# Kernel tuning notes

Hardware: AMD Instinct MI355X
Metric: run time of the kernel (lower is better)

## Reference

```python
import jax, jax.numpy as jnp
import numpy as np

D_IN = 4096
D_OUT = 4096
EPS_NORM = 1e-6
EPS_Q = 1e-8


def _ternary_quantize(w):
    # per-output-channel absmean scale, then round/clamp to {-1,0,1}
    gamma = jnp.mean(jnp.abs(w), axis=-1)
    w_q = jnp.clip(jnp.round(w / (gamma[:, None] + EPS_Q)), -1.0, 1.0)
    return w_q, gamma


def setup_inputs() -> dict:
    key = jax.random.key(0)
    kx, kw = jax.random.split(key)
    x = jax.random.normal(kx, (2, 4096, D_IN), dtype=jnp.float32)
    # kaiming-uniform-like init then ternarize (mirrors torch __init__)
    bound = 1.0 / np.sqrt(D_IN)
    w_init = jax.random.uniform(kw, (D_OUT, D_IN), minval=-bound, maxval=bound, dtype=jnp.float32)
    w_q, gamma = _ternary_quantize(w_init)
    norm_weight = jnp.ones((D_IN,), dtype=jnp.float32)
    return {"x": x, "norm_weight": norm_weight, "w_q": w_q, "gamma": gamma}


def reference(x, norm_weight, w_q, gamma):
    # RMSNorm
    rms = jnp.sqrt(jnp.mean(x * x, axis=-1, keepdims=True) + EPS_NORM)
    xn = x / rms * norm_weight
    # ternary linear (dense fp32 GEMM, math identical to F.linear) + per-channel scale
    y = jnp.einsum('bsd,od->bso', xn, w_q) * gamma
    return y
```

## Files before the change

kernel.cpp:

```cpp
#include <hip/hip_runtime.h>
#include <hip/hip_bf16.h>
#include <stdint.h>

#define D_IN  4096
#define D_OUT 4096
#define MROWS 8192

using i32x4 = __attribute__((ext_vector_type(4))) int;

__global__ __launch_bounds__(256) void prep_kernel(
    const float* __restrict__ x, const float* __restrict__ nw,
    signed char* __restrict__ xq, float* __restrict__ srow,
    const float* __restrict__ wq, signed char* __restrict__ wb) {
  const int b = blockIdx.x;
  const int t = threadIdx.x;

  if (b < MROWS) {
    const float4* xr  = (const float4*)(x + (size_t)b * D_IN);
    const float4* nw4 = (const float4*)nw;

    float4 p[4];
    float ss = 0.f, mx = 0.f;
#pragma unroll
    for (int i = 0; i < 4; ++i) {
      const float4 v = xr[i * 256 + t];
      const float4 w = nw4[i * 256 + t];
      ss += v.x * v.x + v.y * v.y + v.z * v.z + v.w * v.w;
      p[i].x = v.x * w.x; p[i].y = v.y * w.y;
      p[i].z = v.z * w.z; p[i].w = v.w * w.w;
      mx = fmaxf(mx, fmaxf(fmaxf(fabsf(p[i].x), fabsf(p[i].y)),
                           fmaxf(fabsf(p[i].z), fabsf(p[i].w))));
    }
#pragma unroll
    for (int off = 32; off > 0; off >>= 1) {
      ss += __shfl_down(ss, off, 64);
      mx = fmaxf(mx, __shfl_down(mx, off, 64));
    }

    __shared__ float rs[4], rm[4];
    if ((t & 63) == 0) { rs[t >> 6] = ss; rm[t >> 6] = mx; }
    __syncthreads();
    const float scale =
        rsqrtf((rs[0] + rs[1] + rs[2] + rs[3]) * (1.0f / D_IN) + 1e-6f);
    const float rowmax = fmaxf(fmaxf(rm[0], rm[1]), fmaxf(rm[2], rm[3])) * scale;
    const float s   = fmaxf(rowmax, 1e-20f) * (1.0f / 127.0f);
    const float f   = scale / s;
    if (t == 0) srow[b] = s;

    int* out = (int*)(xq + (size_t)b * D_IN);
#pragma unroll
    for (int i = 0; i < 4; ++i) {
      const int q0 = (int)rintf(p[i].x * f);
      const int q1 = (int)rintf(p[i].y * f);
      const int q2 = (int)rintf(p[i].z * f);
      const int q3 = (int)rintf(p[i].w * f);
      out[i * 256 + t] =
          (q0 & 0xFF) | ((q1 & 0xFF) << 8) | ((q2 & 0xFF) << 16) | (q3 << 24);
    }
  } else {
    const int cb = b - MROWS;
    const float4* w4 = (const float4*)wq;
    int* o = (int*)wb;
#pragma unroll
    for (int i = 0; i < 4; ++i) {
      const int idx = cb * 1024 + i * 256 + t;
      const float4 v = w4[idx];
      const int q0 = (int)v.x, q1 = (int)v.y, q2 = (int)v.z, q3 = (int)v.w;
      o[idx] = (q0 & 0xFF) | ((q1 & 0xFF) << 8) | ((q2 & 0xFF) << 16) | (q3 << 24);
    }
  }
}

#define BM 256
#define BN 256
#define BKB 64
#define NKT (D_IN / BKB)
#define SLOT_BYTES (BM * BKB)

#define WVM(n_) asm volatile("s_waitcnt vmcnt(" #n_ ")" ::: "memory")
#define BAR()   __builtin_amdgcn_s_barrier()

#define STAGE(t_, s_)                                                         \
  do {                                                                        \
    const int _k0 = (t_) * BKB;                                               \
    _Pragma("unroll") for (int _i = 0; _i < 2; ++_i)                          \
        __builtin_amdgcn_global_load_lds(                                     \
            (__attribute__((address_space(1))) void*)(A + aOff[_i] + _k0),    \
            (__attribute__((address_space(3))) void*)&sA[s_][ldsOff[_i]],     \
            16, 0, 0);                                                        \
    _Pragma("unroll") for (int _i = 0; _i < 2; ++_i)                          \
        __builtin_amdgcn_global_load_lds(                                     \
            (__attribute__((address_space(1))) void*)(B + bOff[_i] + _k0),    \
            (__attribute__((address_space(3))) void*)&sB[s_][ldsOff[_i]],     \
            16, 0, 0);                                                        \
  } while (0)

#define COMPUTE(s_)                                                           \
  do {                                                                        \
    i32x4 af[8], bfr[4];                                                      \
    _Pragma("unroll") for (int _i = 0; _i < 8; ++_i)                          \
        af[_i] = *(const i32x4*)&sA[s_][aoff + _i * (16 * BKB)];              \
    _Pragma("unroll") for (int _j = 0; _j < 4; ++_j)                          \
        bfr[_j] = *(const i32x4*)&sB[s_][boff + _j * (16 * BKB)];             \
    __builtin_amdgcn_s_setprio(1);                                            \
    _Pragma("unroll") for (int _i = 0; _i < 8; ++_i)                          \
        _Pragma("unroll") for (int _j = 0; _j < 4; ++_j)                      \
            acc[_i][_j] = __builtin_amdgcn_mfma_i32_16x16x64_i8(              \
                af[_i], bfr[_j], acc[_i][_j], 0, 0, 0);                       \
    __builtin_amdgcn_s_setprio(0);                                            \
  } while (0)

__global__ __launch_bounds__(512, 2) void gemm_kernel(
    const signed char* __restrict__ A,
    const signed char* __restrict__ B,
    const float* __restrict__ srow,
    const float* __restrict__ gamma,
    float* __restrict__ C) {
  __shared__ __align__(16) signed char sA[4][SLOT_BYTES];
  __shared__ __align__(16) signed char sB[4][SLOT_BYTES];

  const int tid  = threadIdx.x;
  const int lane = tid & 63;
  const int wv   = tid >> 6;
  const int wm   = wv >> 2;
  const int wn   = wv & 3;
  const int bn   = blockIdx.x;
  const int bm   = blockIdx.y;

  i32x4 acc[8][4];
#pragma unroll
  for (int i = 0; i < 8; ++i)
#pragma unroll
    for (int j = 0; j < 4; ++j) acc[i][j] = (i32x4){0, 0, 0, 0};

  size_t aOff[2], bOff[2];
  int ldsOff[2];
#pragma unroll
  for (int i = 0; i < 2; ++i) {
    const int c  = i * 512 + tid;
    const int r  = c >> 2;
    const int cc = ((c & 3) ^ ((r >> 1) & 3)) * 16;
    aOff[i] = (size_t)(bm * BM + r) * D_IN + cc;
    bOff[i] = (size_t)(bn * BN + r) * D_IN + cc;
    ldsOff[i] = (i * 512 + wv * 64) * 16;
  }

  const int kk   = (((lane >> 4) ^ ((lane >> 1) & 3))) * 16;
  const int aoff = (wm * 128 + (lane & 15)) * BKB + kk;
  const int boff = (wn * 64  + (lane & 15)) * BKB + kk;

  STAGE(0, 0);
  STAGE(1, 1);
  STAGE(2, 2);
  WVM(8);
  BAR();

#pragma unroll 1
  for (int t4 = 0; t4 < NKT - 4; t4 += 4) {
    STAGE(t4 + 3, 3); COMPUTE(0); WVM(8); BAR();
    STAGE(t4 + 4, 0); COMPUTE(1); WVM(8); BAR();
    STAGE(t4 + 5, 1); COMPUTE(2); WVM(8); BAR();
    STAGE(t4 + 6, 2); COMPUTE(3); WVM(8); BAR();
  }
  STAGE(NKT - 1, 3); COMPUTE(0); WVM(8); BAR();
  COMPUTE(1); WVM(4); BAR();
  COMPUTE(2); WVM(0); BAR();
  COMPUTE(3);

  const int col0 = bn * BN + wn * 64 + (lane & 15);
  const int row0 = bm * BM + wm * 128 + ((lane >> 4) * 4);
  float g[4];
#pragma unroll
  for (int j = 0; j < 4; ++j) g[j] = gamma[col0 + j * 16];

#pragma unroll
  for (int i = 0; i < 8; ++i) {
#pragma unroll
    for (int r = 0; r < 4; ++r) {
      const int row = row0 + i * 16 + r;
      const float sr = srow[row];
#pragma unroll
      for (int j = 0; j < 4; ++j) {
        C[(size_t)row * D_OUT + col0 + j * 16] =
            (float)acc[i][j][r] * sr * g[j];
      }
    }
  }
}

#undef STAGE
#undef COMPUTE
#undef WVM
#undef BAR

extern "C" void kernel_launch(void* const* d_in, const int* in_sizes, int n_in,
                              void* d_out, int out_size, void* d_ws, size_t ws_size,
                              hipStream_t stream) {
  const float* x     = (const float*)d_in[0];
  const float* nw    = (const float*)d_in[1];
  const float* wq    = (const float*)d_in[2];
  const float* gamma = (const float*)d_in[3];
  float* y = (float*)d_out;

  signed char* xq = (signed char*)d_ws;
  signed char* wb = xq + (size_t)MROWS * D_IN;
  float* srow = (float*)(wb + (size_t)D_OUT * D_IN);

  prep_kernel<<<MROWS + 4096, 256, 0, stream>>>(x, nw, xq, srow, wq, wb);

  gemm_kernel<<<dim3(D_OUT / BN, MROWS / BM), 512, 0, stream>>>(xq, wb, srow, gamma, y);
}
```

Baseline: 388.0 us.

## Switch GEMM to 3-stage LDS ring with split-phase reads and interleaved loads

Replaces the 4-slot, 4x-unrolled prefetch pipeline with a 3-slot rotating ring. Each k-tile is split into two halves, with LDS fragment reads, A/B global-to-LDS loads and barriers interleaved between the two MFMA halves. This cuts LDS use from 128KB to 96KB per block and spreads memory issue across the compute phase. The cost is one less stage of prefetch depth, four barriers per tile instead of one, and runtime slot indices in place of constant ones.

```diff
diff --git a/kernel.cpp b/kernel.cpp
--- a/kernel.cpp
+++ b/kernel.cpp
@@ -80,34 +80,61 @@
 #define WVM(n_) asm volatile("s_waitcnt vmcnt(" #n_ ")" ::: "memory")
 #define BAR()   __builtin_amdgcn_s_barrier()
 
-#define STAGE(t_, s_)                                                         \
-  do {                                                                        \
-    const int _k0 = (t_) * BKB;                                               \
+#define STG_A(k0_, ss_)                                                       \
+  do {                                                                        \
     _Pragma("unroll") for (int _i = 0; _i < 2; ++_i)                          \
         __builtin_amdgcn_global_load_lds(                                     \
-            (__attribute__((address_space(1))) void*)(A + aOff[_i] + _k0),    \
-            (__attribute__((address_space(3))) void*)&sA[s_][ldsOff[_i]],     \
+            (__attribute__((address_space(1))) void*)(A + aOff[_i] + (k0_)),  \
+            (__attribute__((address_space(3))) void*)&sA[ss_][ldsOff[_i]],    \
             16, 0, 0);                                                        \
+  } while (0)
+#define STG_B(k0_, ss_)                                                       \
+  do {                                                                        \
     _Pragma("unroll") for (int _i = 0; _i < 2; ++_i)                          \
         __builtin_amdgcn_global_load_lds(                                     \
-            (__attribute__((address_space(1))) void*)(B + bOff[_i] + _k0),    \
-            (__attribute__((address_space(3))) void*)&sB[s_][ldsOff[_i]],     \
+            (__attribute__((address_space(1))) void*)(B + bOff[_i] + (k0_)),  \
+            (__attribute__((address_space(3))) void*)&sB[ss_][ldsOff[_i]],    \
             16, 0, 0);                                                        \
   } while (0)
 
-#define COMPUTE(s_)                                                           \
-  do {                                                                        \
-    i32x4 af[8], bfr[4];                                                      \
-    _Pragma("unroll") for (int _i = 0; _i < 8; ++_i)                          \
-        af[_i] = *(const i32x4*)&sA[s_][aoff + _i * (16 * BKB)];              \
+#define READ_P1()                                                             \
+  do {                                                                        \
+    _Pragma("unroll") for (int _i = 0; _i < 4; ++_i)                          \
+        af[_i] = *(const i32x4*)&sA[sC][aoff + _i * (16 * BKB)];              \
     _Pragma("unroll") for (int _j = 0; _j < 4; ++_j)                          \
-        bfr[_j] = *(const i32x4*)&sB[s_][boff + _j * (16 * BKB)];             \
+        bf[_j] = *(const i32x4*)&sB[sC][boff + _j * (16 * BKB)];              \
+  } while (0)
+#define READ_P2()                                                             \
+  do {                                                                        \
+    _Pragma("unroll") for (int _i = 0; _i < 4; ++_i)                          \
+        af[4 + _i] = *(const i32x4*)&sA[sC][aoff + (4 + _i) * (16 * BKB)];    \
+  } while (0)
+
+#define MFMA_HALF(base_)                                                      \
+  do {                                                                        \
     __builtin_amdgcn_s_setprio(1);                                            \
-    _Pragma("unroll") for (int _i = 0; _i < 8; ++_i)                          \
+    _Pragma("unroll") for (int _i = 0; _i < 4; ++_i)                          \
         _Pragma("unroll") for (int _j = 0; _j < 4; ++_j)                      \
-            acc[_i][_j] = __builtin_amdgcn_mfma_i32_16x16x64_i8(              \
-                af[_i], bfr[_j], acc[_i][_j], 0, 0, 0);                       \
+            acc[(base_) + _i][_j] = __builtin_amdgcn_mfma_i32_16x16x64_i8(    \
+                af[(base_) + _i], bf[_j], acc[(base_) + _i][_j], 0, 0, 0);    \
     __builtin_amdgcn_s_setprio(0);                                            \
+  } while (0)
+
+#define TILE_BODY(STGA_, STGB_, WAIT_)                                        \
+  do {                                                                        \
+    i32x4 af[8], bf[4];                                                       \
+    READ_P1();                                                                \
+    STGA_;                                                                    \
+    BAR();                                                                    \
+    MFMA_HALF(0);                                                             \
+    BAR();                                                                    \
+    READ_P2();                                                                \
+    STGB_;                                                                    \
+    BAR();                                                                    \
+    MFMA_HALF(4);                                                             \
+    WAIT_;                                                                    \
+    BAR();                                                                    \
+    const int _t = sC; sC = sN; sN = sS; sS = _t;                             \
   } while (0)
 
 __global__ __launch_bounds__(512, 2) void gemm_kernel(
@@ -116,8 +143,8 @@
     const float* __restrict__ srow,
     const float* __restrict__ gamma,
     float* __restrict__ C) {
-  __shared__ __align__(16) signed char sA[4][SLOT_BYTES];
-  __shared__ __align__(16) signed char sB[4][SLOT_BYTES];
+  __shared__ __align__(16) signed char sA[3][SLOT_BYTES];
+  __shared__ __align__(16) signed char sB[3][SLOT_BYTES];
 
   const int tid  = threadIdx.x;
   const int lane = tid & 63;
@@ -149,23 +176,20 @@
   const int aoff = (wm * 128 + (lane & 15)) * BKB + kk;
   const int boff = (wn * 64  + (lane & 15)) * BKB + kk;
 
-  STAGE(0, 0);
-  STAGE(1, 1);
-  STAGE(2, 2);
-  WVM(8);
+  int sC = 0, sN = 1, sS = 2;
+
+  STG_A(0, 0); STG_B(0, 0);
+  STG_A(BKB, 1); STG_B(BKB, 1);
+  WVM(4);
   BAR();
 
 #pragma unroll 1
-  for (int t4 = 0; t4 < NKT - 4; t4 += 4) {
-    STAGE(t4 + 3, 3); COMPUTE(0); WVM(8); BAR();
-    STAGE(t4 + 4, 0); COMPUTE(1); WVM(8); BAR();
-    STAGE(t4 + 5, 1); COMPUTE(2); WVM(8); BAR();
-    STAGE(t4 + 6, 2); COMPUTE(3); WVM(8); BAR();
-  }
-  STAGE(NKT - 1, 3); COMPUTE(0); WVM(8); BAR();
-  COMPUTE(1); WVM(4); BAR();
-  COMPUTE(2); WVM(0); BAR();
-  COMPUTE(3);
+  for (int T = 0; T < NKT - 2; ++T) {
+    const int k2 = (T + 2) * BKB;
+    TILE_BODY(STG_A(k2, sS), STG_B(k2, sS), WVM(4));
+  }
+  TILE_BODY(, , WVM(0));
+  TILE_BODY(, , );
 
   const int col0 = bn * BN + wn * 64 + (lane & 15);
   const int row0 = bm * BM + wm * 128 + ((lane >> 4) * 4);
@@ -188,8 +212,12 @@
   }
 }
 
-#undef STAGE
-#undef COMPUTE
+#undef TILE_BODY
+#undef MFMA_HALF
+#undef READ_P1
+#undef READ_P2
+#undef STG_A
+#undef STG_B
 #undef WVM
 #undef BAR
 
```

Measured after the change: 425.9 us. 9.8% more time.

## Widen K tile to 128 bytes with double-buffered LDS pipeline

Applied to the files above, without the earlier changes.

Doubles the K-step per stage to 128 int8 values and replaces the 4-slot, 3-deep prefetch pipeline with a 2-slot double buffer that waits for all loads (vmcnt 0) every iteration. The LDS swizzle is changed to an 8-way XOR pattern to match the wider rows. The aim is to halve the number of barriers and loop iterations per K tile. In exchange, prefetch depth drops from about three tiles to one, and the full wait each iteration can expose global load latency.

```diff
diff --git a/kernel.cpp b/kernel.cpp
--- a/kernel.cpp
+++ b/kernel.cpp
@@ -73,40 +73,40 @@
 
 #define BM 256
 #define BN 256
-#define BKB 64
+#define BKB 128
 #define NKT (D_IN / BKB)
 #define SLOT_BYTES (BM * BKB)
 
 #define WVM(n_) asm volatile("s_waitcnt vmcnt(" #n_ ")" ::: "memory")
 #define BAR()   __builtin_amdgcn_s_barrier()
 
-#define STAGE(t_, s_)                                                         \
+#define STAGE(k0_, ss_)                                                       \
   do {                                                                        \
-    const int _k0 = (t_) * BKB;                                               \
-    _Pragma("unroll") for (int _i = 0; _i < 2; ++_i)                          \
+    _Pragma("unroll") for (int _i = 0; _i < 4; ++_i)                          \
         __builtin_amdgcn_global_load_lds(                                     \
-            (__attribute__((address_space(1))) void*)(A + aOff[_i] + _k0),    \
-            (__attribute__((address_space(3))) void*)&sA[s_][ldsOff[_i]],     \
+            (__attribute__((address_space(1))) void*)(A + aOff[_i] + (k0_)),  \
+            (__attribute__((address_space(3))) void*)&sA[ss_][ldsOff[_i]],    \
             16, 0, 0);                                                        \
-    _Pragma("unroll") for (int _i = 0; _i < 2; ++_i)                          \
+    _Pragma("unroll") for (int _i = 0; _i < 4; ++_i)                          \
         __builtin_amdgcn_global_load_lds(                                     \
-            (__attribute__((address_space(1))) void*)(B + bOff[_i] + _k0),    \
-            (__attribute__((address_space(3))) void*)&sB[s_][ldsOff[_i]],     \
+            (__attribute__((address_space(1))) void*)(B + bOff[_i] + (k0_)),  \
+            (__attribute__((address_space(3))) void*)&sB[ss_][ldsOff[_i]],    \
             16, 0, 0);                                                        \
   } while (0)
 
-#define COMPUTE(s_)                                                           \
+#define COMPUTE_K(s_, kk_)                                                    \
   do {                                                                        \
-    i32x4 af[8], bfr[4];                                                      \
+    i32x4 af[8], bf[4];                                                       \
+    const int _ks = (((kk_)*4 + kx) ^ sx) * 16;                               \
     _Pragma("unroll") for (int _i = 0; _i < 8; ++_i)                          \
-        af[_i] = *(const i32x4*)&sA[s_][aoff + _i * (16 * BKB)];              \
+        af[_i] = *(const i32x4*)&sA[s_][aoff0 + _i * (16 * BKB) + _ks];       \
     _Pragma("unroll") for (int _j = 0; _j < 4; ++_j)                          \
-        bfr[_j] = *(const i32x4*)&sB[s_][boff + _j * (16 * BKB)];             \
+        bf[_j] = *(const i32x4*)&sB[s_][boff0 + _j * (16 * BKB) + _ks];       \
     __builtin_amdgcn_s_setprio(1);                                            \
     _Pragma("unroll") for (int _i = 0; _i < 8; ++_i)                          \
         _Pragma("unroll") for (int _j = 0; _j < 4; ++_j)                      \
             acc[_i][_j] = __builtin_amdgcn_mfma_i32_16x16x64_i8(              \
-                af[_i], bfr[_j], acc[_i][_j], 0, 0, 0);                       \
+                af[_i], bf[_j], acc[_i][_j], 0, 0, 0);                        \
     __builtin_amdgcn_s_setprio(0);                                            \
   } while (0)
 
@@ -116,8 +116,8 @@
     const float* __restrict__ srow,
     const float* __restrict__ gamma,
     float* __restrict__ C) {
-  __shared__ __align__(16) signed char sA[4][SLOT_BYTES];
-  __shared__ __align__(16) signed char sB[4][SLOT_BYTES];
+  __shared__ __align__(16) signed char sA[2][SLOT_BYTES];
+  __shared__ __align__(16) signed char sB[2][SLOT_BYTES];
 
   const int tid  = threadIdx.x;
   const int lane = tid & 63;
@@ -133,39 +133,39 @@
 #pragma unroll
     for (int j = 0; j < 4; ++j) acc[i][j] = (i32x4){0, 0, 0, 0};
 
-  size_t aOff[2], bOff[2];
-  int ldsOff[2];
-#pragma unroll
-  for (int i = 0; i < 2; ++i) {
+  size_t aOff[4], bOff[4];
+  int ldsOff[4];
+#pragma unroll
+  for (int i = 0; i < 4; ++i) {
     const int c  = i * 512 + tid;
-    const int r  = c >> 2;
-    const int cc = ((c & 3) ^ ((r >> 1) & 3)) * 16;
+    const int r  = c >> 3;
+    const int j  = c & 7;
+    const int cc = ((j ^ (r & 7)) * 16);
     aOff[i] = (size_t)(bm * BM + r) * D_IN + cc;
     bOff[i] = (size_t)(bn * BN + r) * D_IN + cc;
     ldsOff[i] = (i * 512 + wv * 64) * 16;
   }
 
-  const int kk   = (((lane >> 4) ^ ((lane >> 1) & 3))) * 16;
-  const int aoff = (wm * 128 + (lane & 15)) * BKB + kk;
-  const int boff = (wn * 64  + (lane & 15)) * BKB + kk;
+  const int kx = lane >> 4;
+  const int sx = lane & 7;
+  const int aoff0 = (wm * 128 + (lane & 15)) * BKB;
+  const int boff0 = (wn * 64  + (lane & 15)) * BKB;
 
   STAGE(0, 0);
-  STAGE(1, 1);
-  STAGE(2, 2);
-  WVM(8);
+  WVM(0);
   BAR();
 
 #pragma unroll 1
-  for (int t4 = 0; t4 < NKT - 4; t4 += 4) {
-    STAGE(t4 + 3, 3); COMPUTE(0); WVM(8); BAR();
-    STAGE(t4 + 4, 0); COMPUTE(1); WVM(8); BAR();
-    STAGE(t4 + 5, 1); COMPUTE(2); WVM(8); BAR();
-    STAGE(t4 + 6, 2); COMPUTE(3); WVM(8); BAR();
-  }
-  STAGE(NKT - 1, 3); COMPUTE(0); WVM(8); BAR();
-  COMPUTE(1); WVM(4); BAR();
-  COMPUTE(2); WVM(0); BAR();
-  COMPUTE(3);
+  for (int T = 0; T < NKT - 1; ++T) {
+    const int s = T & 1;
+    STAGE((T + 1) * BKB, s ^ 1);
+    COMPUTE_K(s, 0);
+    COMPUTE_K(s, 1);
+    WVM(0);
+    BAR();
+  }
+  COMPUTE_K((NKT - 1) & 1, 0);
+  COMPUTE_K((NKT - 1) & 1, 1);
 
   const int col0 = bn * BN + wn * 64 + (lane & 15);
   const int row0 = bm * BM + wm * 128 + ((lane >> 4) * 4);
@@ -189,7 +189,7 @@
 }
 
 #undef STAGE
-#undef COMPUTE
+#undef COMPUTE_K
 #undef WVM
 #undef BAR
 
```

Result: slower. 399.8 us (+3.0%).

## Load GEMM B fragments directly into registers, drop B shared-memory staging

Applied to the files above, without the earlier changes.

The int8 GEMM no longer stages the weight (B) tile through LDS. Each wave now reads its B fragments straight from global memory into double-buffered registers, one k-step ahead. The A tile keeps its 4-slot global-to-LDS DMA pipeline. This halves LDS footprint and removes the LDS reads for B, but each B tile is now fetched once per wave row instead of once per block, which adds global/L2 traffic. It also drops the explicit vmcnt waits inside the loop and relies on compiler-inserted waits, so the LDS DMA ordering becomes implicit.

```diff
diff --git a/kernel.cpp b/kernel.cpp
--- a/kernel.cpp
+++ b/kernel.cpp
@@ -78,36 +78,38 @@
 #define SLOT_BYTES (BM * BKB)
 
 #define WVM(n_) asm volatile("s_waitcnt vmcnt(" #n_ ")" ::: "memory")
-#define BAR()   __builtin_amdgcn_s_barrier()
-
-#define STAGE(t_, s_)                                                         \
+
+#define STAGEA(t_)                                                            \
   do {                                                                        \
-    const int _k0 = (t_) * BKB;                                               \
     _Pragma("unroll") for (int _i = 0; _i < 2; ++_i)                          \
         __builtin_amdgcn_global_load_lds(                                     \
-            (__attribute__((address_space(1))) void*)(A + aOff[_i] + _k0),    \
-            (__attribute__((address_space(3))) void*)&sA[s_][ldsOff[_i]],     \
-            16, 0, 0);                                                        \
-    _Pragma("unroll") for (int _i = 0; _i < 2; ++_i)                          \
-        __builtin_amdgcn_global_load_lds(                                     \
-            (__attribute__((address_space(1))) void*)(B + bOff[_i] + _k0),    \
-            (__attribute__((address_space(3))) void*)&sB[s_][ldsOff[_i]],     \
+            (__attribute__((address_space(1))) void*)(A + aOff[_i] +          \
+                                                      (t_) * BKB),            \
+            (__attribute__((address_space(3))) void*)&sA[(t_) & 3]            \
+                                                       [ldsOff[_i]],          \
             16, 0, 0);                                                        \
   } while (0)
 
-#define COMPUTE(s_)                                                           \
+#define LOADB(t_, bf_)                                                        \
   do {                                                                        \
-    i32x4 af[8], bfr[4];                                                      \
+    _Pragma("unroll") for (int _j = 0; _j < 4; ++_j)                          \
+        bf_[_j] = *(const i32x4*)(Bp[_j] + (t_) * BKB);                       \
+  } while (0)
+
+#define BODY(T_, bfC_, LDB_, STG_)                                            \
+  do {                                                                        \
+    i32x4 af[8];                                                              \
     _Pragma("unroll") for (int _i = 0; _i < 8; ++_i)                          \
-        af[_i] = *(const i32x4*)&sA[s_][aoff + _i * (16 * BKB)];              \
-    _Pragma("unroll") for (int _j = 0; _j < 4; ++_j)                          \
-        bfr[_j] = *(const i32x4*)&sB[s_][boff + _j * (16 * BKB)];             \
+        af[_i] = *(const i32x4*)&sA[(T_) & 3][aoff0 + _i * (16 * BKB)];       \
+    LDB_;                                                                     \
+    STG_;                                                                     \
     __builtin_amdgcn_s_setprio(1);                                            \
     _Pragma("unroll") for (int _i = 0; _i < 8; ++_i)                          \
         _Pragma("unroll") for (int _j = 0; _j < 4; ++_j)                      \
             acc[_i][_j] = __builtin_amdgcn_mfma_i32_16x16x64_i8(              \
-                af[_i], bfr[_j], acc[_i][_j], 0, 0, 0);                       \
+                af[_i], bfC_[_j], acc[_i][_j], 0, 0, 0);                      \
     __builtin_amdgcn_s_setprio(0);                                            \
+    __builtin_amdgcn_s_barrier();                                             \
   } while (0)
 
 __global__ __launch_bounds__(512, 2) void gemm_kernel(
@@ -117,7 +119,6 @@
     const float* __restrict__ gamma,
     float* __restrict__ C) {
   __shared__ __align__(16) signed char sA[4][SLOT_BYTES];
-  __shared__ __align__(16) signed char sB[4][SLOT_BYTES];
 
   const int tid  = threadIdx.x;
   const int lane = tid & 63;
@@ -133,7 +134,7 @@
 #pragma unroll
     for (int j = 0; j < 4; ++j) acc[i][j] = (i32x4){0, 0, 0, 0};
 
-  size_t aOff[2], bOff[2];
+  size_t aOff[2];
   int ldsOff[2];
 #pragma unroll
   for (int i = 0; i < 2; ++i) {
@@ -141,31 +142,45 @@
     const int r  = c >> 2;
     const int cc = ((c & 3) ^ ((r >> 1) & 3)) * 16;
     aOff[i] = (size_t)(bm * BM + r) * D_IN + cc;
-    bOff[i] = (size_t)(bn * BN + r) * D_IN + cc;
     ldsOff[i] = (i * 512 + wv * 64) * 16;
   }
 
-  const int kk   = (((lane >> 4) ^ ((lane >> 1) & 3))) * 16;
-  const int aoff = (wm * 128 + (lane & 15)) * BKB + kk;
-  const int boff = (wn * 64  + (lane & 15)) * BKB + kk;
-
-  STAGE(0, 0);
-  STAGE(1, 1);
-  STAGE(2, 2);
+  const int kk    = (((lane >> 4) ^ ((lane >> 1) & 3))) * 16;
+  const int aoff0 = (wm * 128 + (lane & 15)) * BKB + kk;
+
+  const signed char* Bp[4];
+#pragma unroll
+  for (int j = 0; j < 4; ++j)
+    Bp[j] = B + (size_t)(bn * BN + wn * 64 + (lane & 15) + j * 16) * D_IN +
+            (lane >> 4) * 16;
+
+  i32x4 bf0[4], bf1[4];
+
+  STAGEA(0); STAGEA(1); STAGEA(2);
+  LOADB(0, bf0);
   WVM(8);
-  BAR();
+  __builtin_amdgcn_s_barrier();
 
 #pragma unroll 1
-  for (int t4 = 0; t4 < NKT - 4; t4 += 4) {
-    STAGE(t4 + 3, 3); COMPUTE(0); WVM(8); BAR();
-    STAGE(t4 + 4, 0); COMPUTE(1); WVM(8); BAR();
-    STAGE(t4 + 5, 1); COMPUTE(2); WVM(8); BAR();
-    STAGE(t4 + 6, 2); COMPUTE(3); WVM(8); BAR();
-  }
-  STAGE(NKT - 1, 3); COMPUTE(0); WVM(8); BAR();
-  COMPUTE(1); WVM(4); BAR();
-  COMPUTE(2); WVM(0); BAR();
-  COMPUTE(3);
+  for (int TT = 0; TT < NKT - 4; TT += 2) {
+    BODY(TT,     bf0, LOADB(TT + 1, bf1), STAGEA(TT + 3));
+    BODY(TT + 1, bf1, LOADB(TT + 2, bf0), STAGEA(TT + 4));
+  }
+  BODY(60, bf0, LOADB(61, bf1), STAGEA(63));
+  BODY(61, bf1, LOADB(62, bf0), );
+  BODY(62, bf0, LOADB(63, bf1), );
+  {
+    i32x4 af[8];
+#pragma unroll
+    for (int i = 0; i < 8; ++i)
+      af[i] = *(const i32x4*)&sA[63 & 3][aoff0 + i * (16 * BKB)];
+#pragma unroll
+    for (int i = 0; i < 8; ++i)
+#pragma unroll
+      for (int j = 0; j < 4; ++j)
+        acc[i][j] = __builtin_amdgcn_mfma_i32_16x16x64_i8(
+            af[i], bf1[j], acc[i][j], 0, 0, 0);
+  }
 
   const int col0 = bn * BN + wn * 64 + (lane & 15);
   const int row0 = bm * BM + wm * 128 + ((lane >> 4) * 4);
@@ -188,10 +203,10 @@
   }
 }
 
-#undef STAGE
-#undef COMPUTE
+#undef BODY
+#undef LOADB
+#undef STAGEA
 #undef WVM
-#undef BAR
 
 extern "C" void kernel_launch(void* const* d_in, const int* in_sizes, int n_in,
                               void* d_out, int out_size, void* d_ws, size_t ws_size,
```

Measured after the change: 448.8 us. 1.16x slower.
